# Performance work log

Hardware: AMD Instinct MI355X
Metric: run time of the kernel (lower is better)

The kernel has to match this reference:

```python
import jax, jax.numpy as jnp
import numpy as np

TEMP = 0.05
EPS = 1e-6


def _l2norm(x):
    return x / jnp.linalg.norm(x, axis=1, keepdims=True)


def setup_inputs() -> dict:
    key = jax.random.key(0)
    k1, k2, k3, k4 = jax.random.split(key, 4)
    B, D = 4096, 768
    return {
        "feat": jax.random.normal(k1, (B, D), dtype=jnp.float32),
        "feat_gen": jax.random.normal(k2, (B, D), dtype=jnp.float32),
        "feat_aug": jax.random.normal(k3, (B, D), dtype=jnp.float32),
        "targets": jax.random.randint(k4, (B,), 0, 100, dtype=jnp.int64),
    }


def reference(feat, feat_gen, feat_aug, targets):
    B = feat.shape[0]
    on = _l2norm(feat)
    gn = _l2norm(feat_gen)
    an = _l2norm(feat_aug)
    # [B, B] exp-similarity matrices
    exp_ori = jnp.exp(on @ on.T / TEMP)
    exp_gen = jnp.exp(on @ gn.T / TEMP)
    exp_aug = jnp.exp(on @ an.T / TEMP)

    same = (targets[:, None] == targets[None, :])  # [B, B] bool, includes diagonal
    same_f = same.astype(exp_ori.dtype)

    # ---- co loss: anchors vs ori+aug columns ----
    oa = exp_ori + exp_aug
    diff_sum_oa = oa.sum(axis=1) - (oa * same_f).sum(axis=1)        # [B]
    denom_co = diff_sum_oa + exp_gen.sum(axis=1) + EPS              # [B]
    term_o = -jnp.log(exp_ori / (exp_ori + denom_co[:, None]) + EPS)
    term_a = -jnp.log(exp_aug / (exp_aug + denom_co[:, None]) + EPS)
    co_loss = ((term_o + term_a) * same_f).sum() / B

    # ---- ad loss: anchors vs gen columns ----
    diff_sum_g = exp_gen.sum(axis=1) - (exp_gen * same_f).sum(axis=1)
    denom_ad = diff_sum_g + exp_aug.sum(axis=1) + exp_ori.sum(axis=1) + EPS
    term_g = -jnp.log(exp_gen / (exp_gen + denom_ad[:, None]) + EPS)
    ad_loss = (term_g * same_f).sum() / B

    return (ad_loss, co_loss)
```

## Files before the change

### kernel.cpp

```cpp
#include <hip/hip_runtime.h>
#include <hip/hip_bf16.h>
#include <math.h>

#define Bn 4096
#define Dd 768
#define INV_T 20.0f
#define EPSF 1e-6f
#define DG 4.8516519541e8f

#define O_S      0
#define O_SMOA   12288
#define O_SMG    16384
#define ZERO_F   20480
#define O_P      20480
#define O_RM     20608
#define LIST_OFF   262144
#define LCAP       (1u << 19)
#define NB_OFF     33554432

typedef __attribute__((ext_vector_type(8))) short sh8;
typedef __attribute__((ext_vector_type(4))) float f32x4;

#define AS1 __attribute__((address_space(1)))
#define AS3 __attribute__((address_space(3)))

static __device__ __forceinline__ void gl_lds16(const void* g, void* l) {
    __builtin_amdgcn_global_load_lds((const AS1 void*)g, (AS3 void*)l, 16, 0, 0);
}

static __device__ __forceinline__ unsigned short f2b(float f) {
    unsigned int u = __float_as_uint(f);
    unsigned int r = (u + 0x7fffu + ((u >> 16) & 1u)) >> 16;
    return (unsigned short)r;
}

__global__ void norm_kernel(const float* f0, const float* f1, const float* f2, unsigned short* nb) {
    int r = blockIdx.x, m = blockIdx.y, tid = threadIdx.x;
    const float* src = (m == 0 ? f0 : (m == 1 ? f1 : f2)) + (size_t)r * Dd;
    float x0 = src[tid], x1 = src[tid + 256], x2 = src[tid + 512];
    float v = x0 * x0 + x1 * x1 + x2 * x2;
    #pragma unroll
    for (int off = 1; off < 64; off <<= 1) v += __shfl_xor(v, off);
    __shared__ float wr[4];
    if ((tid & 63) == 0) wr[tid >> 6] = v;
    __syncthreads();
    float inv = rsqrtf(wr[0] + wr[1] + wr[2] + wr[3]);
    unsigned short* dst = nb + ((size_t)m * Bn + r) * Dd;
    dst[tid] = f2b(x0 * inv);
    dst[tid + 256] = f2b(x1 * inv);
    dst[tid + 512] = f2b(x2 * inv);
}

__launch_bounds__(1024)
__global__ void sort_kernel(const int* tg, unsigned int* I, float* out) {
    float* F = (float*)I;
    __shared__ unsigned int h[128], pb[128], cur[128];
    int tid = threadIdx.x;
    for (int e = tid; e < ZERO_F; e += 1024) F[e] = 0.f;
    if (tid == 0) { out[0] = 0.f; out[1] = 0.f; }
    if (tid < 128) { h[tid] = 0; cur[tid] = 0; }
    __syncthreads();
    for (int e = tid; e < Bn; e += 1024) atomicAdd(&h[tg[e]], 1u);
    __syncthreads();
    if (tid < 128) pb[tid] = h[tid] * h[tid];
    __syncthreads();
    for (int s = 1; s < 128; s <<= 1) {
        unsigned int b = 0;
        if (tid < 128 && tid >= s) b = pb[tid - s];
        __syncthreads();
        if (tid < 128) pb[tid] += b;
        __syncthreads();
    }
    if (tid == 127) I[O_P] = pb[127];
    uint2* RM = (uint2*)(I + O_RM);
    for (int e = tid; e < Bn; e += 1024) {
        int c = tg[e];
        unsigned int r = atomicAdd(&cur[c], 1u);
        unsigned int n = h[c];
        RM[e] = make_uint2((unsigned)c | (r << 8), (pb[c] - n * n) + r * n);
    }
}

__launch_bounds__(256)
__global__ void gemm_rowsum(const unsigned short* nb, char* ws) {
    float* F = (float*)ws;
    const unsigned int* I = (const unsigned int*)ws;
    const uint2* RM = (const uint2*)(I + O_RM);
    int z = blockIdx.z;
    const unsigned short* Ag = nb;
    const unsigned short* Bg = nb + (size_t)z * Bn * Dd;
    int m0 = blockIdx.y * 128, n0 = blockIdx.x * 128;
    int tid = threadIdx.x, lane = tid & 63, wave = tid >> 6;
    int wm = (wave >> 1) * 64, wn = (wave & 1) * 64;
    int lid = lane & 15, q = lane >> 4;
    __shared__ __align__(16) unsigned short Asm[128 * 32];
    __shared__ __align__(16) unsigned short Bsm[128 * 32];
    int c0 = tid, c1 = tid + 256;
    int row0 = c0 >> 2, sg0 = (c0 & 3) ^ ((row0 >> 1) & 3);
    int row1 = c1 >> 2, sg1 = (c1 & 3) ^ ((row1 >> 1) & 3);
    const unsigned short* gA0 = Ag + (size_t)(m0 + row0) * Dd + sg0 * 8;
    const unsigned short* gA1 = Ag + (size_t)(m0 + row1) * Dd + sg1 * 8;
    const unsigned short* gB0 = Bg + (size_t)(n0 + row0) * Dd + sg0 * 8;
    const unsigned short* gB1 = Bg + (size_t)(n0 + row1) * Dd + sg1 * 8;
    unsigned short* lA0 = &Asm[c0 * 8];
    unsigned short* lA1 = &Asm[c1 * 8];
    unsigned short* lB0 = &Bsm[c0 * 8];
    unsigned short* lB1 = &Bsm[c1 * 8];
    f32x4 acc[4][4] = {};
    for (int kt = 0; kt < Dd / 32; ++kt) {
        __syncthreads();
        gl_lds16(gA0 + kt * 32, lA0);
        gl_lds16(gA1 + kt * 32, lA1);
        gl_lds16(gB0 + kt * 32, lB0);
        gl_lds16(gB1 + kt * 32, lB1);
        __syncthreads();
        sh8 af[4], bf[4];
        #pragma unroll
        for (int i = 0; i < 4; ++i) {
            int r = wm + i * 16 + lid;
            af[i] = *(const sh8*)&Asm[r * 32 + ((q ^ ((r >> 1) & 3)) * 8)];
        }
        #pragma unroll
        for (int j = 0; j < 4; ++j) {
            int r = wn + j * 16 + lid;
            bf[j] = *(const sh8*)&Bsm[r * 32 + ((q ^ ((r >> 1) & 3)) * 8)];
        }
        #pragma unroll
        for (int i = 0; i < 4; ++i)
            #pragma unroll
            for (int j = 0; j < 4; ++j)
                acc[i][j] = __builtin_amdgcn_mfma_f32_16x16x32_bf16(af[i], bf[j], acc[i][j], 0, 0, 0);
    }
    unsigned int rmc[4];
    #pragma unroll
    for (int j = 0; j < 4; ++j) rmc[j] = RM[n0 + wn + j * 16 + lid].x;
    int smoff = (z == 1) ? O_SMG : O_SMOA;
    unsigned int* Lw = (unsigned int*)(ws + LIST_OFF);
    #pragma unroll
    for (int i = 0; i < 4; ++i)
        #pragma unroll
        for (int reg = 0; reg < 4; ++reg) {
            int grow = m0 + wm + i * 16 + q * 4 + reg;
            uint2 rm = RM[grow];
            unsigned int trow = rm.x & 255u, rsb = rm.y;
            float rs = 0.f, ms = 0.f;
            #pragma unroll
            for (int j = 0; j < 4; ++j) {
                int gcol = n0 + wn + j * 16 + lid;
                float x = acc[i][j][reg] * INV_T;
                float e = __expf(x);
                if (z == 0 && gcol == grow) e = 0.f;
                rs += e;
                if ((rmc[j] & 255u) == trow) {
                    ms += e;
                    unsigned int slot = rsb + (rmc[j] >> 8);
                    if (slot < LCAP) {
                        if (z == 0) {
                            Lw[slot * 4 + 0] = (unsigned)grow;
                            Lw[slot * 4 + 1] = __float_as_uint(x);
                        } else {
                            Lw[slot * 4 + 1 + z] = __float_as_uint(x);
                        }
                    }
                }
            }
            #pragma unroll
            for (int off = 1; off < 16; off <<= 1) {
                rs += __shfl_xor(rs, off);
                ms += __shfl_xor(ms, off);
            }
            if (lid == 0) {
                atomicAdd(&F[O_S + z * Bn + grow], rs);
                atomicAdd(&F[smoff + grow], ms);
            }
        }
}

__launch_bounds__(256)
__global__ void loss_kernel(char* ws, float* out) {
    float* F = (float*)ws;
    const unsigned int* I = (const unsigned int*)ws;
    const uint4* L = (const uint4*)(ws + LIST_OFF);
    unsigned int n = I[O_P]; if (n > LCAP) n = LCAP;
    float a0 = 0.f, a1 = 0.f;
    unsigned int stride = gridDim.x * 256;
    for (unsigned int idx = blockIdx.x * 256 + threadIdx.x; idx < n; idx += stride) {
        uint4 en = L[idx];
        int i = (int)en.x;
        float son = F[O_S + i], sgen = F[O_S + Bn + i], saug = F[O_S + 2 * Bn + i];
        float dco = (son + saug - F[O_SMOA + i]) + sgen + EPSF;
        float dad = (sgen - F[O_SMG + i]) + saug + son + DG + EPSF;
        float eo = __expf(__uint_as_float(en.y));
        float eg = __expf(__uint_as_float(en.z));
        float ea = __expf(__uint_as_float(en.w));
        a0 += -__logf(eg / (eg + dad) + EPSF);
        a1 += -__logf(eo / (eo + dco) + EPSF) - __logf(ea / (ea + dco) + EPSF);
    }
    #pragma unroll
    for (int off = 1; off < 64; off <<= 1) { a0 += __shfl_xor(a0, off); a1 += __shfl_xor(a1, off); }
    __shared__ float r0[4], r1[4];
    int tid = threadIdx.x;
    if ((tid & 63) == 0) { r0[tid >> 6] = a0; r1[tid >> 6] = a1; }
    __syncthreads();
    if (tid == 0) {
        atomicAdd(&out[0], (r0[0] + r0[1] + r0[2] + r0[3]) * (1.0f / Bn));
        atomicAdd(&out[1], (r1[0] + r1[1] + r1[2] + r1[3]) * (1.0f / Bn));
    }
}

extern "C" void kernel_launch(void* const* d_in, const int* in_sizes, int n_in,
                              void* d_out, int out_size, void* d_ws, size_t ws_size,
                              hipStream_t stream) {
    const float* f0 = (const float*)d_in[0];
    const float* f1 = (const float*)d_in[1];
    const float* f2 = (const float*)d_in[2];
    const int* tg = (const int*)d_in[3];
    char* ws = (char*)d_ws;
    unsigned int* I = (unsigned int*)d_ws;
    unsigned short* nb = (unsigned short*)(ws + NB_OFF);
    float* out = (float*)d_out;

    norm_kernel<<<dim3(Bn, 3), 256, 0, stream>>>(f0, f1, f2, nb);
    sort_kernel<<<1, 1024, 0, stream>>>(tg, I, out);
    gemm_rowsum<<<dim3(32, 32, 3), 256, 0, stream>>>(nb, ws);
    loss_kernel<<<256, 256, 0, stream>>>(ws, out);
}
```

Measured before the change: 234.9 us.

## Exploit symmetry of ori-ori Gram matrix and fuse norm with sort

Computes only the upper-triangular tiles of the on·onᵀ GEMM (528 instead of 1024 tiles) and mirrors their contributions into column sums, same-class sums and the pair list for the transposed positions. The sort/histogram kernel is folded into the normalisation launch as an extra grid row, removing one launch. The exp is rewritten as exp2 with a pre-scaled constant. The cost is extra atomics and list writes per symmetric tile, plus a 1D tile index decoded with a small loop.

```diff
diff --git a/kernel.cpp b/kernel.cpp
--- a/kernel.cpp
+++ b/kernel.cpp
@@ -4,7 +4,7 @@
 
 #define Bn 4096
 #define Dd 768
-#define INV_T 20.0f
+#define SC2 28.85390081777927f
 #define EPSF 1e-6f
 #define DG 4.8516519541e8f
 
@@ -34,8 +34,40 @@
     return (unsigned short)r;
 }
 
-__global__ void norm_kernel(const float* f0, const float* f1, const float* f2, unsigned short* nb) {
-    int r = blockIdx.x, m = blockIdx.y, tid = threadIdx.x;
+__global__ void norm_sort_kernel(const float* f0, const float* f1, const float* f2,
+                                 const int* tg, unsigned short* nb,
+                                 unsigned int* I, float* out) {
+    int m = blockIdx.y, tid = threadIdx.x;
+    if (m == 3) {
+        if (blockIdx.x != 0) return;
+        float* F = (float*)I;
+        __shared__ unsigned int h[128], pb[128], cur[128];
+        for (int e = tid; e < ZERO_F; e += 256) F[e] = 0.f;
+        if (tid == 0) { out[0] = 0.f; out[1] = 0.f; }
+        if (tid < 128) { h[tid] = 0; cur[tid] = 0; }
+        __syncthreads();
+        for (int e = tid; e < Bn; e += 256) atomicAdd(&h[tg[e]], 1u);
+        __syncthreads();
+        if (tid < 128) pb[tid] = h[tid] * h[tid];
+        __syncthreads();
+        for (int s = 1; s < 128; s <<= 1) {
+            unsigned int b = 0;
+            if (tid < 128 && tid >= s) b = pb[tid - s];
+            __syncthreads();
+            if (tid < 128) pb[tid] += b;
+            __syncthreads();
+        }
+        if (tid == 127) I[O_P] = pb[127];
+        uint2* RM = (uint2*)(I + O_RM);
+        for (int e = tid; e < Bn; e += 256) {
+            int c = tg[e];
+            unsigned int r = atomicAdd(&cur[c], 1u);
+            unsigned int n = h[c];
+            RM[e] = make_uint2((unsigned)c | (r << 8), (pb[c] - n * n) + r * n);
+        }
+        return;
+    }
+    int r = blockIdx.x;
     const float* src = (m == 0 ? f0 : (m == 1 ? f1 : f2)) + (size_t)r * Dd;
     float x0 = src[tid], x1 = src[tid + 256], x2 = src[tid + 512];
     float v = x0 * x0 + x1 * x1 + x2 * x2;
@@ -51,45 +83,28 @@
     dst[tid + 512] = f2b(x2 * inv);
 }
 
-__launch_bounds__(1024)
-__global__ void sort_kernel(const int* tg, unsigned int* I, float* out) {
-    float* F = (float*)I;
-    __shared__ unsigned int h[128], pb[128], cur[128];
-    int tid = threadIdx.x;
-    for (int e = tid; e < ZERO_F; e += 1024) F[e] = 0.f;
-    if (tid == 0) { out[0] = 0.f; out[1] = 0.f; }
-    if (tid < 128) { h[tid] = 0; cur[tid] = 0; }
-    __syncthreads();
-    for (int e = tid; e < Bn; e += 1024) atomicAdd(&h[tg[e]], 1u);
-    __syncthreads();
-    if (tid < 128) pb[tid] = h[tid] * h[tid];
-    __syncthreads();
-    for (int s = 1; s < 128; s <<= 1) {
-        unsigned int b = 0;
-        if (tid < 128 && tid >= s) b = pb[tid - s];
-        __syncthreads();
-        if (tid < 128) pb[tid] += b;
-        __syncthreads();
-    }
-    if (tid == 127) I[O_P] = pb[127];
-    uint2* RM = (uint2*)(I + O_RM);
-    for (int e = tid; e < Bn; e += 1024) {
-        int c = tg[e];
-        unsigned int r = atomicAdd(&cur[c], 1u);
-        unsigned int n = h[c];
-        RM[e] = make_uint2((unsigned)c | (r << 8), (pb[c] - n * n) + r * n);
-    }
-}
-
 __launch_bounds__(256)
 __global__ void gemm_rowsum(const unsigned short* nb, char* ws) {
     float* F = (float*)ws;
     const unsigned int* I = (const unsigned int*)ws;
     const uint2* RM = (const uint2*)(I + O_RM);
-    int z = blockIdx.z;
+    int id = blockIdx.x;
+    int z, m0, n0;
+    bool sym = false;
+    if (id < 528) {
+        z = 0;
+        int t = id, by = 0;
+        while (t >= 32 - by) { t -= 32 - by; ++by; }
+        int bx = by + t;
+        m0 = by * 128; n0 = bx * 128;
+        sym = (bx != by);
+    } else if (id < 1552) {
+        z = 1; int t = id - 528;  n0 = (t & 31) * 128; m0 = (t >> 5) * 128;
+    } else {
+        z = 2; int t = id - 1552; n0 = (t & 31) * 128; m0 = (t >> 5) * 128;
+    }
     const unsigned short* Ag = nb;
     const unsigned short* Bg = nb + (size_t)z * Bn * Dd;
-    int m0 = blockIdx.y * 128, n0 = blockIdx.x * 128;
     int tid = threadIdx.x, lane = tid & 63, wave = tid >> 6;
     int wm = (wave >> 1) * 64, wn = (wave & 1) * 64;
     int lid = lane & 15, q = lane >> 4;
@@ -131,33 +146,43 @@
             for (int j = 0; j < 4; ++j)
                 acc[i][j] = __builtin_amdgcn_mfma_f32_16x16x32_bf16(af[i], bf[j], acc[i][j], 0, 0, 0);
     }
-    unsigned int rmc[4];
-    #pragma unroll
-    for (int j = 0; j < 4; ++j) rmc[j] = RM[n0 + wn + j * 16 + lid].x;
+    uint2 rmc[4];
+    #pragma unroll
+    for (int j = 0; j < 4; ++j) rmc[j] = RM[n0 + wn + j * 16 + lid];
     int smoff = (z == 1) ? O_SMG : O_SMOA;
     unsigned int* Lw = (unsigned int*)(ws + LIST_OFF);
+    float cs[4] = {0.f, 0.f, 0.f, 0.f}, msc[4] = {0.f, 0.f, 0.f, 0.f};
     #pragma unroll
     for (int i = 0; i < 4; ++i)
         #pragma unroll
         for (int reg = 0; reg < 4; ++reg) {
             int grow = m0 + wm + i * 16 + q * 4 + reg;
             uint2 rm = RM[grow];
-            unsigned int trow = rm.x & 255u, rsb = rm.y;
+            unsigned int trow = rm.x & 255u, rrank = rm.x >> 8, rsb = rm.y;
             float rs = 0.f, ms = 0.f;
             #pragma unroll
             for (int j = 0; j < 4; ++j) {
                 int gcol = n0 + wn + j * 16 + lid;
-                float x = acc[i][j][reg] * INV_T;
-                float e = __expf(x);
+                float x = acc[i][j][reg] * SC2;
+                float e = exp2f(x);
                 if (z == 0 && gcol == grow) e = 0.f;
                 rs += e;
-                if ((rmc[j] & 255u) == trow) {
+                if (sym) cs[j] += e;
+                if ((rmc[j].x & 255u) == trow) {
                     ms += e;
-                    unsigned int slot = rsb + (rmc[j] >> 8);
+                    if (sym) msc[j] += e;
+                    unsigned int slot = rsb + (rmc[j].x >> 8);
                     if (slot < LCAP) {
                         if (z == 0) {
                             Lw[slot * 4 + 0] = (unsigned)grow;
                             Lw[slot * 4 + 1] = __float_as_uint(x);
+                            if (sym) {
+                                unsigned int slot2 = rmc[j].y + rrank;
+                                if (slot2 < LCAP) {
+                                    Lw[slot2 * 4 + 0] = (unsigned)gcol;
+                                    Lw[slot2 * 4 + 1] = __float_as_uint(x);
+                                }
+                            }
                         } else {
                             Lw[slot * 4 + 1 + z] = __float_as_uint(x);
                         }
@@ -174,6 +199,19 @@
                 atomicAdd(&F[smoff + grow], ms);
             }
         }
+    if (sym) {
+        #pragma unroll
+        for (int j = 0; j < 4; ++j) {
+            int gcol = n0 + wn + j * 16 + lid;
+            float c = cs[j], mc = msc[j];
+            c += __shfl_xor(c, 16);  c += __shfl_xor(c, 32);
+            mc += __shfl_xor(mc, 16); mc += __shfl_xor(mc, 32);
+            if (q == 0) {
+                atomicAdd(&F[O_S + gcol], c);
+                atomicAdd(&F[O_SMOA + gcol], mc);
+            }
+        }
+    }
 }
 
 __launch_bounds__(256)
@@ -190,9 +228,9 @@
         float son = F[O_S + i], sgen = F[O_S + Bn + i], saug = F[O_S + 2 * Bn + i];
         float dco = (son + saug - F[O_SMOA + i]) + sgen + EPSF;
         float dad = (sgen - F[O_SMG + i]) + saug + son + DG + EPSF;
-        float eo = __expf(__uint_as_float(en.y));
-        float eg = __expf(__uint_as_float(en.z));
-        float ea = __expf(__uint_as_float(en.w));
+        float eo = exp2f(__uint_as_float(en.y));
+        float eg = exp2f(__uint_as_float(en.z));
+        float ea = exp2f(__uint_as_float(en.w));
         a0 += -__logf(eg / (eg + dad) + EPSF);
         a1 += -__logf(eo / (eo + dco) + EPSF) - __logf(ea / (ea + dco) + EPSF);
     }
@@ -220,8 +258,7 @@
     unsigned short* nb = (unsigned short*)(ws + NB_OFF);
     float* out = (float*)d_out;
 
-    norm_kernel<<<dim3(Bn, 3), 256, 0, stream>>>(f0, f1, f2, nb);
-    sort_kernel<<<1, 1024, 0, stream>>>(tg, I, out);
-    gemm_rowsum<<<dim3(32, 32, 3), 256, 0, stream>>>(nb, ws);
+    norm_sort_kernel<<<dim3(Bn, 4), 256, 0, stream>>>(f0, f1, f2, tg, nb, I, out);
+    gemm_rowsum<<<2576, 256, 0, stream>>>(nb, ws);
     loss_kernel<<<256, 256, 0, stream>>>(ws, out);
 }
```

Measured after the change: 266.7 us. +13.6%, slower.

## Fuse norm, sort, GEMM and loss into one cooperative persistent kernel

Applied to the files above, without the earlier changes.

Merges the four kernels into a single cooperative launch that uses grid-wide syncs between phases. Each persistent block handles a 128x128 output tile and loops over the three B matrices, so the A tile is reused across them. The 8 waves are laid out as 2x4 with 64x32 subtiles, and exp is switched to exp2 with a prescaled constant. The aim is to remove launch overhead and serialization, at the cost of grid.sync latency, smaller per-wave tiles and a fixed grid of persistent blocks.

```diff
diff --git a/kernel.cpp b/kernel.cpp
--- a/kernel.cpp
+++ b/kernel.cpp
@@ -1,10 +1,13 @@
 #include <hip/hip_runtime.h>
 #include <hip/hip_bf16.h>
+#include <hip/hip_cooperative_groups.h>
 #include <math.h>
+
+namespace cg = cooperative_groups;
 
 #define Bn 4096
 #define Dd 768
-#define INV_T 20.0f
+#define SC2 28.85390081777927f
 #define EPSF 1e-6f
 #define DG 4.8516519541e8f
 
@@ -34,177 +37,176 @@
     return (unsigned short)r;
 }
 
-__global__ void norm_kernel(const float* f0, const float* f1, const float* f2, unsigned short* nb) {
-    int r = blockIdx.x, m = blockIdx.y, tid = threadIdx.x;
-    const float* src = (m == 0 ? f0 : (m == 1 ? f1 : f2)) + (size_t)r * Dd;
-    float x0 = src[tid], x1 = src[tid + 256], x2 = src[tid + 512];
-    float v = x0 * x0 + x1 * x1 + x2 * x2;
-    #pragma unroll
-    for (int off = 1; off < 64; off <<= 1) v += __shfl_xor(v, off);
-    __shared__ float wr[4];
-    if ((tid & 63) == 0) wr[tid >> 6] = v;
-    __syncthreads();
-    float inv = rsqrtf(wr[0] + wr[1] + wr[2] + wr[3]);
-    unsigned short* dst = nb + ((size_t)m * Bn + r) * Dd;
-    dst[tid] = f2b(x0 * inv);
-    dst[tid + 256] = f2b(x1 * inv);
-    dst[tid + 512] = f2b(x2 * inv);
-}
-
-__launch_bounds__(1024)
-__global__ void sort_kernel(const int* tg, unsigned int* I, float* out) {
-    float* F = (float*)I;
-    __shared__ unsigned int h[128], pb[128], cur[128];
-    int tid = threadIdx.x;
-    for (int e = tid; e < ZERO_F; e += 1024) F[e] = 0.f;
-    if (tid == 0) { out[0] = 0.f; out[1] = 0.f; }
-    if (tid < 128) { h[tid] = 0; cur[tid] = 0; }
-    __syncthreads();
-    for (int e = tid; e < Bn; e += 1024) atomicAdd(&h[tg[e]], 1u);
-    __syncthreads();
-    if (tid < 128) pb[tid] = h[tid] * h[tid];
-    __syncthreads();
-    for (int s = 1; s < 128; s <<= 1) {
-        unsigned int b = 0;
-        if (tid < 128 && tid >= s) b = pb[tid - s];
-        __syncthreads();
-        if (tid < 128) pb[tid] += b;
-        __syncthreads();
+__global__ __launch_bounds__(512, 4) void mega_kernel(
+        const float* f0, const float* f1, const float* f2, const int* tg,
+        unsigned short* nb, char* ws, float* out) {
+    cg::grid_group grid = cg::this_grid();
+    __shared__ __align__(16) char smem[16384];
+    float* F = (float*)ws;
+    unsigned int* I = (unsigned int*)ws;
+    int b = blockIdx.x, tid = threadIdx.x, G = gridDim.x;
+    int lane = tid & 63, wave = tid >> 6;
+
+    if (b == 0) {
+        for (int e = tid; e < ZERO_F; e += 512) F[e] = 0.f;
+        if (tid == 0) { out[0] = 0.f; out[1] = 0.f; }
+        unsigned int* h = (unsigned int*)smem;
+        unsigned int* pb = h + 128;
+        unsigned int* cur = h + 256;
+        if (tid < 128) { h[tid] = 0; cur[tid] = 0; }
+        __syncthreads();
+        for (int e = tid; e < Bn; e += 512) atomicAdd(&h[tg[e]], 1u);
+        __syncthreads();
+        if (tid < 128) pb[tid] = h[tid] * h[tid];
+        __syncthreads();
+        for (int s = 1; s < 128; s <<= 1) {
+            unsigned int v = 0;
+            if (tid < 128 && tid >= s) v = pb[tid - s];
+            __syncthreads();
+            if (tid < 128) pb[tid] += v;
+            __syncthreads();
+        }
+        if (tid == 127) I[O_P] = pb[127];
+        uint2* RMw = (uint2*)(I + O_RM);
+        for (int e = tid; e < Bn; e += 512) {
+            int c = tg[e];
+            unsigned int r = atomicAdd(&cur[c], 1u);
+            unsigned int n = h[c];
+            RMw[e] = make_uint2((unsigned)c | (r << 8), (pb[c] - n * n) + r * n);
+        }
+    } else {
+        float* wr = (float*)smem;
+        for (int task = b - 1; task < 3 * Bn; task += G - 1) {
+            int m = task >> 12, r = task & (Bn - 1);
+            const float* src = (m == 0 ? f0 : (m == 1 ? f1 : f2)) + (size_t)r * Dd;
+            float x0 = src[tid];
+            float x1 = (tid < 256) ? src[tid + 512] : 0.f;
+            float v = x0 * x0 + x1 * x1;
+            #pragma unroll
+            for (int off = 1; off < 64; off <<= 1) v += __shfl_xor(v, off);
+            if (lane == 0) wr[wave] = v;
+            __syncthreads();
+            float inv = rsqrtf(wr[0] + wr[1] + wr[2] + wr[3] + wr[4] + wr[5] + wr[6] + wr[7]);
+            unsigned short* dst = nb + ((size_t)m * Bn + r) * Dd;
+            dst[tid] = f2b(x0 * inv);
+            if (tid < 256) dst[tid + 512] = f2b(x1 * inv);
+            __syncthreads();
+        }
     }
-    if (tid == 127) I[O_P] = pb[127];
-    uint2* RM = (uint2*)(I + O_RM);
-    for (int e = tid; e < Bn; e += 1024) {
-        int c = tg[e];
-        unsigned int r = atomicAdd(&cur[c], 1u);
-        unsigned int n = h[c];
-        RM[e] = make_uint2((unsigned)c | (r << 8), (pb[c] - n * n) + r * n);
-    }
-}
-
-__launch_bounds__(256)
-__global__ void gemm_rowsum(const unsigned short* nb, char* ws) {
-    float* F = (float*)ws;
-    const unsigned int* I = (const unsigned int*)ws;
+    grid.sync();
+
     const uint2* RM = (const uint2*)(I + O_RM);
-    int z = blockIdx.z;
-    const unsigned short* Ag = nb;
-    const unsigned short* Bg = nb + (size_t)z * Bn * Dd;
-    int m0 = blockIdx.y * 128, n0 = blockIdx.x * 128;
-    int tid = threadIdx.x, lane = tid & 63, wave = tid >> 6;
-    int wm = (wave >> 1) * 64, wn = (wave & 1) * 64;
+    unsigned short* Asm = (unsigned short*)smem;
+    unsigned short* Bsm = Asm + 128 * 32;
+    int wm = (wave >> 2) * 64, wn = (wave & 3) * 32;
     int lid = lane & 15, q = lane >> 4;
-    __shared__ __align__(16) unsigned short Asm[128 * 32];
-    __shared__ __align__(16) unsigned short Bsm[128 * 32];
-    int c0 = tid, c1 = tid + 256;
-    int row0 = c0 >> 2, sg0 = (c0 & 3) ^ ((row0 >> 1) & 3);
-    int row1 = c1 >> 2, sg1 = (c1 & 3) ^ ((row1 >> 1) & 3);
-    const unsigned short* gA0 = Ag + (size_t)(m0 + row0) * Dd + sg0 * 8;
-    const unsigned short* gA1 = Ag + (size_t)(m0 + row1) * Dd + sg1 * 8;
-    const unsigned short* gB0 = Bg + (size_t)(n0 + row0) * Dd + sg0 * 8;
-    const unsigned short* gB1 = Bg + (size_t)(n0 + row1) * Dd + sg1 * 8;
-    unsigned short* lA0 = &Asm[c0 * 8];
-    unsigned short* lA1 = &Asm[c1 * 8];
-    unsigned short* lB0 = &Bsm[c0 * 8];
-    unsigned short* lB1 = &Bsm[c1 * 8];
-    f32x4 acc[4][4] = {};
-    for (int kt = 0; kt < Dd / 32; ++kt) {
-        __syncthreads();
-        gl_lds16(gA0 + kt * 32, lA0);
-        gl_lds16(gA1 + kt * 32, lA1);
-        gl_lds16(gB0 + kt * 32, lB0);
-        gl_lds16(gB1 + kt * 32, lB1);
-        __syncthreads();
-        sh8 af[4], bf[4];
+    int srow = tid >> 2, spos = tid & 3;
+    int sseg = spos ^ ((srow >> 1) & 3);
+    unsigned int* Lw = (unsigned int*)(ws + LIST_OFF);
+    for (int t = b; t < 1024; t += G) {
+        int m0 = (t >> 5) * 128, n0 = (t & 31) * 128;
+        uint2 rmc[2];
         #pragma unroll
-        for (int i = 0; i < 4; ++i) {
-            int r = wm + i * 16 + lid;
-            af[i] = *(const sh8*)&Asm[r * 32 + ((q ^ ((r >> 1) & 3)) * 8)];
-        }
-        #pragma unroll
-        for (int j = 0; j < 4; ++j) {
-            int r = wn + j * 16 + lid;
-            bf[j] = *(const sh8*)&Bsm[r * 32 + ((q ^ ((r >> 1) & 3)) * 8)];
-        }
-        #pragma unroll
-        for (int i = 0; i < 4; ++i)
+        for (int j = 0; j < 2; ++j) rmc[j] = RM[n0 + wn + j * 16 + lid];
+        const unsigned short* gA = nb + (size_t)(m0 + srow) * Dd + sseg * 8;
+        for (int z = 0; z < 3; ++z) {
+            const unsigned short* gB = nb + (size_t)z * Bn * Dd + (size_t)(n0 + srow) * Dd + sseg * 8;
+            f32x4 acc[4][2] = {};
+            for (int kt = 0; kt < Dd / 32; ++kt) {
+                __syncthreads();
+                gl_lds16(gA + kt * 32, &Asm[tid * 8]);
+                gl_lds16(gB + kt * 32, &Bsm[tid * 8]);
+                __syncthreads();
+                sh8 af[4], bf[2];
+                #pragma unroll
+                for (int i = 0; i < 4; ++i) {
+                    int r = wm + i * 16 + lid;
+                    af[i] = *(const sh8*)&Asm[r * 32 + ((q ^ ((r >> 1) & 3)) * 8)];
+                }
+                #pragma unroll
+                for (int j = 0; j < 2; ++j) {
+                    int r = wn + j * 16 + lid;
+                    bf[j] = *(const sh8*)&Bsm[r * 32 + ((q ^ ((r >> 1) & 3)) * 8)];
+                }
+                #pragma unroll
+                for (int i = 0; i < 4; ++i)
+                    #pragma unroll
+                    for (int j = 0; j < 2; ++j)
+                        acc[i][j] = __builtin_amdgcn_mfma_f32_16x16x32_bf16(af[i], bf[j], acc[i][j], 0, 0, 0);
+            }
+            int smoff = (z == 1) ? O_SMG : O_SMOA;
             #pragma unroll
-            for (int j = 0; j < 4; ++j)
-                acc[i][j] = __builtin_amdgcn_mfma_f32_16x16x32_bf16(af[i], bf[j], acc[i][j], 0, 0, 0);
-    }
-    unsigned int rmc[4];
-    #pragma unroll
-    for (int j = 0; j < 4; ++j) rmc[j] = RM[n0 + wn + j * 16 + lid].x;
-    int smoff = (z == 1) ? O_SMG : O_SMOA;
-    unsigned int* Lw = (unsigned int*)(ws + LIST_OFF);
-    #pragma unroll
-    for (int i = 0; i < 4; ++i)
-        #pragma unroll
-        for (int reg = 0; reg < 4; ++reg) {
-            int grow = m0 + wm + i * 16 + q * 4 + reg;
-            uint2 rm = RM[grow];
-            unsigned int trow = rm.x & 255u, rsb = rm.y;
-            float rs = 0.f, ms = 0.f;
-            #pragma unroll
-            for (int j = 0; j < 4; ++j) {
-                int gcol = n0 + wn + j * 16 + lid;
-                float x = acc[i][j][reg] * INV_T;
-                float e = __expf(x);
-                if (z == 0 && gcol == grow) e = 0.f;
-                rs += e;
-                if ((rmc[j] & 255u) == trow) {
-                    ms += e;
-                    unsigned int slot = rsb + (rmc[j] >> 8);
-                    if (slot < LCAP) {
-                        if (z == 0) {
-                            Lw[slot * 4 + 0] = (unsigned)grow;
-                            Lw[slot * 4 + 1] = __float_as_uint(x);
-                        } else {
-                            Lw[slot * 4 + 1 + z] = __float_as_uint(x);
+            for (int i = 0; i < 4; ++i)
+                #pragma unroll
+                for (int reg = 0; reg < 4; ++reg) {
+                    int grow = m0 + wm + i * 16 + q * 4 + reg;
+                    uint2 rm = RM[grow];
+                    unsigned int trow = rm.x & 255u, rsb = rm.y;
+                    float rs = 0.f, ms = 0.f;
+                    #pragma unroll
+                    for (int j = 0; j < 2; ++j) {
+                        int gcol = n0 + wn + j * 16 + lid;
+                        float x = acc[i][j][reg] * SC2;
+                        float e = exp2f(x);
+                        if (z == 0 && gcol == grow) e = 0.f;
+                        rs += e;
+                        if ((rmc[j].x & 255u) == trow) {
+                            ms += e;
+                            unsigned int slot = rsb + (rmc[j].x >> 8);
+                            if (slot < LCAP) {
+                                if (z == 0) {
+                                    Lw[slot * 4 + 0] = (unsigned)grow;
+                                    Lw[slot * 4 + 1] = __float_as_uint(x);
+                                } else {
+                                    Lw[slot * 4 + 1 + z] = __float_as_uint(x);
+                                }
+                            }
                         }
                     }
+                    #pragma unroll
+                    for (int off = 1; off < 16; off <<= 1) {
+                        rs += __shfl_xor(rs, off);
+                        ms += __shfl_xor(ms, off);
+                    }
+                    if (lid == 0) {
+                        atomicAdd(&F[O_S + z * Bn + grow], rs);
+                        atomicAdd(&F[smoff + grow], ms);
+                    }
                 }
-            }
-            #pragma unroll
-            for (int off = 1; off < 16; off <<= 1) {
-                rs += __shfl_xor(rs, off);
-                ms += __shfl_xor(ms, off);
-            }
-            if (lid == 0) {
-                atomicAdd(&F[O_S + z * Bn + grow], rs);
-                atomicAdd(&F[smoff + grow], ms);
-            }
-        }
-}
-
-__launch_bounds__(256)
-__global__ void loss_kernel(char* ws, float* out) {
-    float* F = (float*)ws;
-    const unsigned int* I = (const unsigned int*)ws;
-    const uint4* L = (const uint4*)(ws + LIST_OFF);
-    unsigned int n = I[O_P]; if (n > LCAP) n = LCAP;
-    float a0 = 0.f, a1 = 0.f;
-    unsigned int stride = gridDim.x * 256;
-    for (unsigned int idx = blockIdx.x * 256 + threadIdx.x; idx < n; idx += stride) {
-        uint4 en = L[idx];
-        int i = (int)en.x;
-        float son = F[O_S + i], sgen = F[O_S + Bn + i], saug = F[O_S + 2 * Bn + i];
-        float dco = (son + saug - F[O_SMOA + i]) + sgen + EPSF;
-        float dad = (sgen - F[O_SMG + i]) + saug + son + DG + EPSF;
-        float eo = __expf(__uint_as_float(en.y));
-        float eg = __expf(__uint_as_float(en.z));
-        float ea = __expf(__uint_as_float(en.w));
-        a0 += -__logf(eg / (eg + dad) + EPSF);
-        a1 += -__logf(eo / (eo + dco) + EPSF) - __logf(ea / (ea + dco) + EPSF);
+        }
     }
-    #pragma unroll
-    for (int off = 1; off < 64; off <<= 1) { a0 += __shfl_xor(a0, off); a1 += __shfl_xor(a1, off); }
-    __shared__ float r0[4], r1[4];
-    int tid = threadIdx.x;
-    if ((tid & 63) == 0) { r0[tid >> 6] = a0; r1[tid >> 6] = a1; }
-    __syncthreads();
-    if (tid == 0) {
-        atomicAdd(&out[0], (r0[0] + r0[1] + r0[2] + r0[3]) * (1.0f / Bn));
-        atomicAdd(&out[1], (r1[0] + r1[1] + r1[2] + r1[3]) * (1.0f / Bn));
+    grid.sync();
+
+    {
+        const uint4* L = (const uint4*)(ws + LIST_OFF);
+        unsigned int n = I[O_P]; if (n > LCAP) n = LCAP;
+        float a0 = 0.f, a1 = 0.f;
+        unsigned int stride = (unsigned int)G * 512u;
+        for (unsigned int idx = b * 512 + tid; idx < n; idx += stride) {
+            uint4 en = L[idx];
+            int i = (int)en.x;
+            float son = F[O_S + i], sgen = F[O_S + Bn + i], saug = F[O_S + 2 * Bn + i];
+            float dco = (son + saug - F[O_SMOA + i]) + sgen + EPSF;
+            float dad = (sgen - F[O_SMG + i]) + saug + son + DG + EPSF;
+            float eo = exp2f(__uint_as_float(en.y));
+            float eg = exp2f(__uint_as_float(en.z));
+            float ea = exp2f(__uint_as_float(en.w));
+            a0 += -__logf(eg / (eg + dad) + EPSF);
+            a1 += -__logf(eo / (eo + dco) + EPSF) - __logf(ea / (ea + dco) + EPSF);
+        }
+        #pragma unroll
+        for (int off = 1; off < 64; off <<= 1) { a0 += __shfl_xor(a0, off); a1 += __shfl_xor(a1, off); }
+        float* r0 = (float*)smem;
+        float* r1 = r0 + 8;
+        __syncthreads();
+        if (lane == 0) { r0[wave] = a0; r1[wave] = a1; }
+        __syncthreads();
+        if (tid == 0) {
+            float s0 = r0[0] + r0[1] + r0[2] + r0[3] + r0[4] + r0[5] + r0[6] + r0[7];
+            float s1 = r1[0] + r1[1] + r1[2] + r1[3] + r1[4] + r1[5] + r1[6] + r1[7];
+            atomicAdd(&out[0], s0 * (1.0f / Bn));
+            atomicAdd(&out[1], s1 * (1.0f / Bn));
+        }
     }
 }
 
@@ -216,12 +218,15 @@
     const float* f2 = (const float*)d_in[2];
     const int* tg = (const int*)d_in[3];
     char* ws = (char*)d_ws;
-    unsigned int* I = (unsigned int*)d_ws;
     unsigned short* nb = (unsigned short*)(ws + NB_OFF);
     float* out = (float*)d_out;
 
-    norm_kernel<<<dim3(Bn, 3), 256, 0, stream>>>(f0, f1, f2, nb);
-    sort_kernel<<<1, 1024, 0, stream>>>(tg, I, out);
-    gemm_rowsum<<<dim3(32, 32, 3), 256, 0, stream>>>(nb, ws);
-    loss_kernel<<<256, 256, 0, stream>>>(ws, out);
-}
+    int occ = 0;
+    (void)hipOccupancyMaxActiveBlocksPerMultiprocessor(&occ, (const void*)mega_kernel, 512, 0);
+    int G = (occ >= 2) ? 512 : 256;
+
+    void* args[] = { (void*)&f0, (void*)&f1, (void*)&f2, (void*)&tg,
+                     (void*)&nb, (void*)&ws, (void*)&out };
+    hipLaunchCooperativeKernel((const void*)mega_kernel, dim3(G), dim3(512),
+                               args, 0, stream);
+}
```

Measured after the change: 486.6 us. +107.2%, slower.

## Switch similarity GEMM to FP8 e4m3 scaled MFMA with 128-wide K tiles

Applied to the files above, without the earlier changes.

Normalized features are quantized to FP8 e4m3 instead of bf16, and the GEMM uses the scaled f8f6f4 16x16x128 MFMA with 128-byte K tiles and an XOR swizzle. The norm kernel is vectorized with float4 loads, and exp is computed as exp2 with a folded log2(e)/T scale. This aims to halve operand bandwidth and raise matrix throughput. The trade is a large precision loss, because the logits are scaled by 1/T before exponentiation.

```diff
diff --git a/kernel.cpp b/kernel.cpp
--- a/kernel.cpp
+++ b/kernel.cpp
@@ -4,7 +4,7 @@
 
 #define Bn 4096
 #define Dd 768
-#define INV_T 20.0f
+#define SC2 28.85390081777927f
 #define EPSF 1e-6f
 #define DG 4.8516519541e8f
 
@@ -18,8 +18,8 @@
 #define LCAP       (1u << 19)
 #define NB_OFF     33554432
 
-typedef __attribute__((ext_vector_type(8))) short sh8;
 typedef __attribute__((ext_vector_type(4))) float f32x4;
+typedef __attribute__((ext_vector_type(8))) int i32x8;
 
 #define AS1 __attribute__((address_space(1)))
 #define AS3 __attribute__((address_space(3)))
@@ -28,27 +28,45 @@
     __builtin_amdgcn_global_load_lds((const AS1 void*)g, (AS3 void*)l, 16, 0, 0);
 }
 
-static __device__ __forceinline__ unsigned short f2b(float f) {
+static __device__ __forceinline__ unsigned int f2e4m3(float f) {
     unsigned int u = __float_as_uint(f);
-    unsigned int r = (u + 0x7fffu + ((u >> 16) & 1u)) >> 16;
-    return (unsigned short)r;
-}
-
-__global__ void norm_kernel(const float* f0, const float* f1, const float* f2, unsigned short* nb) {
+    unsigned int sign = (u >> 24) & 0x80u;
+    int exp = (int)((u >> 23) & 0xffu) - 127;
+    unsigned int man = u & 0x7fffffu;
+    if (exp >= -6) {
+        unsigned int mant = man >> 20;
+        unsigned int rest = man & 0xfffffu;
+        unsigned int v = ((unsigned int)(exp + 7) << 3) | mant;
+        if (rest > 0x80000u || (rest == 0x80000u && (v & 1u))) v++;
+        return sign | v;
+    }
+    if (exp <= -11) return sign;
+    int rs = 20 + (-6 - exp);
+    unsigned int full = 0x800000u | man;
+    unsigned int mant = full >> rs;
+    unsigned int rest = full & ((1u << rs) - 1u);
+    unsigned int half = 1u << (rs - 1);
+    if (rest > half || (rest == half && (mant & 1u))) mant++;
+    return sign | mant;
+}
+
+__global__ void norm_kernel(const float* f0, const float* f1, const float* f2, unsigned char* nb) {
     int r = blockIdx.x, m = blockIdx.y, tid = threadIdx.x;
     const float* src = (m == 0 ? f0 : (m == 1 ? f1 : f2)) + (size_t)r * Dd;
-    float x0 = src[tid], x1 = src[tid + 256], x2 = src[tid + 512];
-    float v = x0 * x0 + x1 * x1 + x2 * x2;
+    float4 x = make_float4(0.f, 0.f, 0.f, 0.f);
+    if (tid < 192) x = ((const float4*)src)[tid];
+    float v = x.x * x.x + x.y * x.y + x.z * x.z + x.w * x.w;
     #pragma unroll
     for (int off = 1; off < 64; off <<= 1) v += __shfl_xor(v, off);
     __shared__ float wr[4];
     if ((tid & 63) == 0) wr[tid >> 6] = v;
     __syncthreads();
     float inv = rsqrtf(wr[0] + wr[1] + wr[2] + wr[3]);
-    unsigned short* dst = nb + ((size_t)m * Bn + r) * Dd;
-    dst[tid] = f2b(x0 * inv);
-    dst[tid + 256] = f2b(x1 * inv);
-    dst[tid + 512] = f2b(x2 * inv);
+    if (tid < 192) {
+        unsigned int p = f2e4m3(x.x * inv) | (f2e4m3(x.y * inv) << 8) |
+                         (f2e4m3(x.z * inv) << 16) | (f2e4m3(x.w * inv) << 24);
+        ((unsigned int*)(nb + ((size_t)m * Bn + r) * Dd))[tid] = p;
+    }
 }
 
 __launch_bounds__(1024)
@@ -82,58 +100,59 @@
 }
 
 __launch_bounds__(256)
-__global__ void gemm_rowsum(const unsigned short* nb, char* ws) {
+__global__ void gemm_rowsum(const unsigned char* nb, char* ws) {
     float* F = (float*)ws;
     const unsigned int* I = (const unsigned int*)ws;
     const uint2* RM = (const uint2*)(I + O_RM);
     int z = blockIdx.z;
-    const unsigned short* Ag = nb;
-    const unsigned short* Bg = nb + (size_t)z * Bn * Dd;
+    const unsigned char* Ag = nb;
+    const unsigned char* Bg = nb + (size_t)z * Bn * Dd;
     int m0 = blockIdx.y * 128, n0 = blockIdx.x * 128;
     int tid = threadIdx.x, lane = tid & 63, wave = tid >> 6;
     int wm = (wave >> 1) * 64, wn = (wave & 1) * 64;
     int lid = lane & 15, q = lane >> 4;
-    __shared__ __align__(16) unsigned short Asm[128 * 32];
-    __shared__ __align__(16) unsigned short Bsm[128 * 32];
-    int c0 = tid, c1 = tid + 256;
-    int row0 = c0 >> 2, sg0 = (c0 & 3) ^ ((row0 >> 1) & 3);
-    int row1 = c1 >> 2, sg1 = (c1 & 3) ^ ((row1 >> 1) & 3);
-    const unsigned short* gA0 = Ag + (size_t)(m0 + row0) * Dd + sg0 * 8;
-    const unsigned short* gA1 = Ag + (size_t)(m0 + row1) * Dd + sg1 * 8;
-    const unsigned short* gB0 = Bg + (size_t)(n0 + row0) * Dd + sg0 * 8;
-    const unsigned short* gB1 = Bg + (size_t)(n0 + row1) * Dd + sg1 * 8;
-    unsigned short* lA0 = &Asm[c0 * 8];
-    unsigned short* lA1 = &Asm[c1 * 8];
-    unsigned short* lB0 = &Bsm[c0 * 8];
-    unsigned short* lB1 = &Bsm[c1 * 8];
+    __shared__ __align__(16) unsigned char Asm[128 * 128];
+    __shared__ __align__(16) unsigned char Bsm[128 * 128];
+    int crow[4], cgs[4];
+    #pragma unroll
+    for (int s = 0; s < 4; ++s) {
+        int c = tid + s * 256;
+        crow[s] = c >> 3;
+        cgs[s] = (c & 7) ^ (crow[s] & 7);
+    }
     f32x4 acc[4][4] = {};
-    for (int kt = 0; kt < Dd / 32; ++kt) {
-        __syncthreads();
-        gl_lds16(gA0 + kt * 32, lA0);
-        gl_lds16(gA1 + kt * 32, lA1);
-        gl_lds16(gB0 + kt * 32, lB0);
-        gl_lds16(gB1 + kt * 32, lB1);
-        __syncthreads();
-        sh8 af[4], bf[4];
+    for (int kt = 0; kt < Dd / 128; ++kt) {
+        __syncthreads();
+        #pragma unroll
+        for (int s = 0; s < 4; ++s) {
+            int c = tid + s * 256;
+            gl_lds16(Ag + (size_t)(m0 + crow[s]) * Dd + kt * 128 + cgs[s] * 16, &Asm[c * 16]);
+            gl_lds16(Bg + (size_t)(n0 + crow[s]) * Dd + kt * 128 + cgs[s] * 16, &Bsm[c * 16]);
+        }
+        __syncthreads();
+        i32x8 af[4];
         #pragma unroll
         for (int i = 0; i < 4; ++i) {
             int r = wm + i * 16 + lid;
-            af[i] = *(const sh8*)&Asm[r * 32 + ((q ^ ((r >> 1) & 3)) * 8)];
+            int4 lo = *(const int4*)&Asm[r * 128 + (((q * 2 + 0) ^ (r & 7)) * 16)];
+            int4 hi = *(const int4*)&Asm[r * 128 + (((q * 2 + 1) ^ (r & 7)) * 16)];
+            af[i] = (i32x8){lo.x, lo.y, lo.z, lo.w, hi.x, hi.y, hi.z, hi.w};
         }
         #pragma unroll
         for (int j = 0; j < 4; ++j) {
             int r = wn + j * 16 + lid;
-            bf[j] = *(const sh8*)&Bsm[r * 32 + ((q ^ ((r >> 1) & 3)) * 8)];
-        }
-        #pragma unroll
-        for (int i = 0; i < 4; ++i)
+            int4 lo = *(const int4*)&Bsm[r * 128 + (((q * 2 + 0) ^ (r & 7)) * 16)];
+            int4 hi = *(const int4*)&Bsm[r * 128 + (((q * 2 + 1) ^ (r & 7)) * 16)];
+            i32x8 bf = (i32x8){lo.x, lo.y, lo.z, lo.w, hi.x, hi.y, hi.z, hi.w};
             #pragma unroll
-            for (int j = 0; j < 4; ++j)
-                acc[i][j] = __builtin_amdgcn_mfma_f32_16x16x32_bf16(af[i], bf[j], acc[i][j], 0, 0, 0);
-    }
-    unsigned int rmc[4];
-    #pragma unroll
-    for (int j = 0; j < 4; ++j) rmc[j] = RM[n0 + wn + j * 16 + lid].x;
+            for (int i = 0; i < 4; ++i)
+                acc[i][j] = __builtin_amdgcn_mfma_scale_f32_16x16x128_f8f6f4(
+                    af[i], bf, acc[i][j], 0, 0, 0, 0x7f7f7f7f, 0, 0x7f7f7f7f);
+        }
+    }
+    uint2 rmc[4];
+    #pragma unroll
+    for (int j = 0; j < 4; ++j) rmc[j] = RM[n0 + wn + j * 16 + lid];
     int smoff = (z == 1) ? O_SMG : O_SMOA;
     unsigned int* Lw = (unsigned int*)(ws + LIST_OFF);
     #pragma unroll
@@ -147,13 +166,13 @@
             #pragma unroll
             for (int j = 0; j < 4; ++j) {
                 int gcol = n0 + wn + j * 16 + lid;
-                float x = acc[i][j][reg] * INV_T;
-                float e = __expf(x);
+                float x = acc[i][j][reg] * SC2;
+                float e = exp2f(x);
                 if (z == 0 && gcol == grow) e = 0.f;
                 rs += e;
-                if ((rmc[j] & 255u) == trow) {
+                if ((rmc[j].x & 255u) == trow) {
                     ms += e;
-                    unsigned int slot = rsb + (rmc[j] >> 8);
+                    unsigned int slot = rsb + (rmc[j].x >> 8);
                     if (slot < LCAP) {
                         if (z == 0) {
                             Lw[slot * 4 + 0] = (unsigned)grow;
@@ -190,9 +209,9 @@
         float son = F[O_S + i], sgen = F[O_S + Bn + i], saug = F[O_S + 2 * Bn + i];
         float dco = (son + saug - F[O_SMOA + i]) + sgen + EPSF;
         float dad = (sgen - F[O_SMG + i]) + saug + son + DG + EPSF;
-        float eo = __expf(__uint_as_float(en.y));
-        float eg = __expf(__uint_as_float(en.z));
-        float ea = __expf(__uint_as_float(en.w));
+        float eo = exp2f(__uint_as_float(en.y));
+        float eg = exp2f(__uint_as_float(en.z));
+        float ea = exp2f(__uint_as_float(en.w));
         a0 += -__logf(eg / (eg + dad) + EPSF);
         a1 += -__logf(eo / (eo + dco) + EPSF) - __logf(ea / (ea + dco) + EPSF);
     }
@@ -217,7 +236,7 @@
     const int* tg = (const int*)d_in[3];
     char* ws = (char*)d_ws;
     unsigned int* I = (unsigned int*)d_ws;
-    unsigned short* nb = (unsigned short*)(ws + NB_OFF);
+    unsigned char* nb = (unsigned char*)(ws + NB_OFF);
     float* out = (float*)d_out;
 
     norm_kernel<<<dim3(Bn, 3), 256, 0, stream>>>(f0, f1, f2, nb);
```

Result: slower. 312.6 us (+33.1%).
